# Kernel tuning notes

Hardware: AMD Instinct MI355X
Metric: run time of the kernel (lower is better)

## Reference

```python
import jax, jax.numpy as jnp
import numpy as np

T = 2048          # tokens (flattened prefill)
H = 3584          # hidden_size
NH = 16           # num query heads
NKV = 8           # num kv heads
G = NH // NKV     # GQA group size
D = 256           # head_dim
SCALE = 256.0 ** -0.5   # query_pre_attn_scalar ** -0.5
WINDOW = 1024     # sliding_window_size
CAP = 50.0        # logit softcap
BASE = 10000.0    # rope theta
NEG = -1e30


def _rope(x, positions):
    # x: [T, n, D], neox-style rotary over full head_dim
    half = D // 2
    inv_freq = 1.0 / (BASE ** (jnp.arange(0, D, 2, dtype=jnp.float32) / D))  # [half]
    ang = positions.astype(jnp.float32)[:, None] * inv_freq  # [T, half]
    cos = jnp.cos(ang)[:, None, :]  # [T,1,half]
    sin = jnp.sin(ang)[:, None, :]
    x1, x2 = x[..., :half], x[..., half:]
    return jnp.concatenate([x1 * cos - x2 * sin, x2 * cos + x1 * sin], axis=-1)


def setup_inputs() -> dict:
    key = jax.random.key(0)
    ks = jax.random.split(key, 5)
    s = 0.02
    return {
        "hidden_states": jax.random.normal(ks[0], (T, H), dtype=jnp.float32),
        "Wq": jax.random.normal(ks[1], (H, NH * D), dtype=jnp.float32) * s,
        "Wk": jax.random.normal(ks[2], (H, NKV * D), dtype=jnp.float32) * s,
        "Wv": jax.random.normal(ks[3], (H, NKV * D), dtype=jnp.float32) * s,
        "Wo": jax.random.normal(ks[4], (NH * D, H), dtype=jnp.float32) * s,
        "positions": jnp.arange(T, dtype=jnp.int32),
    }


def reference(hidden_states, Wq, Wk, Wv, Wo, positions):
    q = (hidden_states @ Wq).reshape(T, NH, D)
    k = (hidden_states @ Wk).reshape(T, NKV, D)
    v = (hidden_states @ Wv).reshape(T, NKV, D)
    q = _rope(q, positions)
    k = _rope(k, positions)

    # GQA attention: group query heads over kv heads
    qg = (q * SCALE).reshape(T, NKV, G, D)
    scores = jnp.einsum('qhgd,khd->hgqk', qg, k)  # [NKV,G,T,T]
    scores = CAP * jnp.tanh(scores / CAP)         # logit softcap

    i = jnp.arange(T)[:, None]
    j = jnp.arange(T)[None, :]
    mask = (j <= i) & (i - j < WINDOW)            # causal + sliding window
    scores = jnp.where(mask, scores, NEG)

    p = jax.nn.softmax(scores, axis=-1)
    o = jnp.einsum('hgqk,khd->qhgd', p, v).reshape(T, NH * D)
    return o @ Wo
```

## Files before the change

kernel.cpp:

```cpp
#include <hip/hip_runtime.h>
#include <math.h>

typedef __attribute__((ext_vector_type(8))) __bf16 bf16x8;
typedef __attribute__((ext_vector_type(4))) __bf16 bf16x4;
typedef __attribute__((ext_vector_type(4))) float f32x4;

#define TSEQ 2048
#define HDIM 3584
#define NQH  16
#define NKVH 8
#define DH   256
#define WIN  1024
#define QKD  (NQH * DH)
#define KVD  (NKVH * DH)
#define QKVN 8192

#define MFMA __builtin_amdgcn_mfma_f32_16x16x32_bf16

__device__ __forceinline__ void gload_lds16(const void* g, void* l) {
  __builtin_amdgcn_global_load_lds(
      (const __attribute__((address_space(1))) void*)g,
      (__attribute__((address_space(3))) void*)l, 16, 0, 0);
}


__global__ void cvt_bf16_kernel(const float* __restrict__ in,
                                __bf16* __restrict__ out, long n) {
  long i = ((long)blockIdx.x * blockDim.x + threadIdx.x) * 4;
  if (i >= n) return;
  float4 v = *reinterpret_cast<const float4*>(in + i);
  bf16x4 o4;
  o4.x = (__bf16)v.x; o4.y = (__bf16)v.y; o4.z = (__bf16)v.z; o4.w = (__bf16)v.w;
  *reinterpret_cast<bf16x4*>(out + i) = o4;
}

__global__ void transpose_cvt64_kernel(const float* __restrict__ in,
                                       __bf16* __restrict__ out, int R, int C) {
  __shared__ float tile[64][65];
  const int tid = threadIdx.x;
  const int r0 = blockIdx.y * 64, c0 = blockIdx.x * 64;
#pragma unroll
  for (int it = 0; it < 4; ++it) {
    int f = tid + it * 256;
    int row = f >> 4, c4 = (f & 15) * 4;
    float4 v = *reinterpret_cast<const float4*>(&in[(size_t)(r0 + row) * C + c0 + c4]);
    tile[row][c4] = v.x; tile[row][c4 + 1] = v.y;
    tile[row][c4 + 2] = v.z; tile[row][c4 + 3] = v.w;
  }
  __syncthreads();
#pragma unroll
  for (int it = 0; it < 2; ++it) {
    int s = tid + it * 256;
    int oc = s >> 3, rb = (s & 7) * 8;
    bf16x8 o8;
#pragma unroll
    for (int j = 0; j < 8; ++j) o8[j] = (__bf16)tile[rb + j][oc];
    *reinterpret_cast<bf16x8*>(&out[(size_t)(c0 + oc) * R + r0 + rb]) = o8;
  }
}

__global__ void transpose_bf16_kernel(const __bf16* __restrict__ in,
                                      __bf16* __restrict__ out, int ldin, int ldout) {
  __shared__ __bf16 tile[32][33];
  const int tx = threadIdx.x, ty = threadIdx.y;
  const int c0 = blockIdx.x * 32, r0 = blockIdx.y * 32;
#pragma unroll
  for (int i = 0; i < 4; ++i)
    tile[ty + i * 8][tx] = in[(size_t)(r0 + ty + i * 8) * ldin + (c0 + tx)];
  __syncthreads();
#pragma unroll
  for (int i = 0; i < 4; ++i)
    out[(size_t)(c0 + ty + i * 8) * ldout + (r0 + tx)] = tile[tx][ty + i * 8];
}

__global__ void rope_table_kernel(const int* __restrict__ positions,
                                  float* __restrict__ ct,
                                  float* __restrict__ st) {
  int i = blockIdx.x * blockDim.x + threadIdx.x;
  if (i >= TSEQ * 128) return;
  int t = i >> 7, j = i & 127;
  float invf = (float)exp((double)(-2 * j) * (9.210340371976184 / 256.0));
  float ang = (float)positions[t] * invf;
  ct[i] = cosf(ang);
  st[i] = sinf(ang);
}

__global__ void rope_apply_kernel(__bf16* __restrict__ x,
                                  const float* __restrict__ ct,
                                  const float* __restrict__ st,
                                  int heads, int ld, float scale, int total) {
  int i = blockIdx.x * blockDim.x + threadIdx.x;
  if (i >= total) return;
  int j = i & 127;
  int th = i >> 7;
  int t = th / heads;
  int head = th - t * heads;
  size_t base = (size_t)t * ld + head * DH + j;
  float x1 = (float)x[base], x2 = (float)x[base + 128];
  float c = ct[(t << 7) + j], s = st[(t << 7) + j];
  x[base]       = (__bf16)((x1 * c - x2 * s) * scale);
  x[base + 128] = (__bf16)((x2 * c + x1 * s) * scale);
}

__global__ void reduce2_kernel(const float* __restrict__ p0,
                               const float* __restrict__ p1,
                               float* __restrict__ out, int n4) {
  int stride = gridDim.x * blockDim.x;
  for (int i = blockIdx.x * blockDim.x + threadIdx.x; i < n4; i += stride) {
    float4 a = reinterpret_cast<const float4*>(p0)[i];
    float4 b = reinterpret_cast<const float4*>(p1)[i];
    a.x += b.x; a.y += b.y; a.z += b.z; a.w += b.w;
    reinterpret_cast<float4*>(out)[i] = a;
  }
}


__device__ __forceinline__ void stage_half(const __bf16* __restrict__ gbase,
                                           int row0, int ldg, int k0,
                                           __bf16* lds_half, int tid) {
  const int lane = tid & 63;
  const int w = tid >> 6;
  const int lr = lane >> 3;
  const int swzcol = ((lane & 7) ^ lr) << 3;
  const __bf16* g = gbase + (size_t)(row0 + w * 8 + lr) * ldg + k0 + swzcol;
  __bf16* l = lds_half + w * 512;
  gload_lds16(g, l);
  gload_lds16(g + (size_t)64 * ldg, l + 4096);
}

#define BAR __builtin_amdgcn_s_barrier()

#define RD_A(DST, BASE, MO)                                         \
  _Pragma("unroll")                                                 \
  for (int m_ = 0; m_ < 4; ++m_) {                                  \
    const __bf16* p_ = (BASE) + (((MO) + m_) * 16 + l15) * 64;      \
    DST[m_][0] = *(const bf16x8*)(p_ + kxa);                        \
    DST[m_][1] = *(const bf16x8*)(p_ + kxb);                        \
  }

#define RD_B(DST, BASE, NO)                                         \
  _Pragma("unroll")                                                 \
  for (int n_ = 0; n_ < 2; ++n_) {                                  \
    const __bf16* p_ = (BASE) + (bro + ((NO) + n_) * 16 + l15) * 64;\
    DST[n_][0] = *(const bf16x8*)(p_ + kxa);                        \
    DST[n_][1] = *(const bf16x8*)(p_ + kxb);                        \
  }

#define MQUAD(AF, BF, MO, NO)                                          \
  __builtin_amdgcn_s_setprio(1);                                       \
  _Pragma("unroll")                                                    \
  for (int m_ = 0; m_ < 4; ++m_)                                       \
    _Pragma("unroll")                                                  \
    for (int n_ = 0; n_ < 2; ++n_) {                                   \
      acc[(MO) + m_][(NO) + n_] =                                      \
          MFMA(AF[m_][0], BF[n_][0], acc[(MO) + m_][(NO) + n_], 0, 0, 0); \
      acc[(MO) + m_][(NO) + n_] =                                      \
          MFMA(AF[m_][1], BF[n_][1], acc[(MO) + m_][(NO) + n_], 0, 0, 0); \
    }                                                                  \
  __builtin_amdgcn_s_setprio(0);

template <typename CT>
__global__ __launch_bounds__(512, 2) void gemm256_kernel(
    const __bf16* __restrict__ A, const __bf16* __restrict__ B,
    CT* __restrict__ C, int lda, int Klen, int ldc, int nrc, size_t cstride) {
  __shared__ __bf16 lds[2][2][2][8192];

  const int nwg = gridDim.x;
  const int per = nwg >> 3;
  const int wg = (blockIdx.x & 7) * per + (blockIdx.x >> 3);
  const int kslice = wg / nrc;
  const int rem = wg - kslice * nrc;
  const int row0 = (rem & 7) * 256;
  const int col0 = (rem >> 3) * 256;
  const int k0 = kslice * Klen;
  CT* Cs = C + (size_t)kslice * cstride;

  const int tid = threadIdx.x;
  const int lane = tid & 63, w = tid >> 6;
  const int wr = w >> 2, wc = w & 3;
  const int l15 = lane & 15, lg = lane >> 4;
  const int swz = (lane & 7) << 3;
  const int kxa = (lg * 8) ^ swz;
  const int kxb = (32 + lg * 8) ^ swz;
  const int bro = (wc & 1) * 64;

  const __bf16* Ablk = A + (size_t)row0 * lda + k0;
  const __bf16* Bblk = B + (size_t)col0 * lda + k0;

  const __bf16* Ae = &lds[0][0][wr][0];
  const __bf16* Be = &lds[0][1][wc >> 1][0];
  const __bf16* Ao = &lds[1][0][wr][0];
  const __bf16* Bo = &lds[1][1][wc >> 1][0];

  f32x4 acc[8][4] = {};
  const int NT = Klen >> 6;
  const int NI = NT >> 1;

  stage_half(Ablk, 0,   lda, 0,  &lds[0][0][0][0], tid);
  stage_half(Ablk, 128, lda, 0,  &lds[0][0][1][0], tid);
  stage_half(Bblk, 0,   lda, 0,  &lds[0][1][0][0], tid);
  stage_half(Bblk, 128, lda, 0,  &lds[0][1][1][0], tid);
  stage_half(Ablk, 0,   lda, 64, &lds[1][0][0][0], tid);
  stage_half(Ablk, 128, lda, 64, &lds[1][0][1][0], tid);
  asm volatile("s_waitcnt vmcnt(4)" ::: "memory");
  BAR;

  bf16x8 a03[4][2], a47[4][2], b01[2][2], b23[2][2];

  for (int j = 0; j < NI; ++j) {
    const int e = 2 * j, o = 2 * j + 1;
    const bool last = (j == NI - 1);

    RD_A(a03, Ae, 0);
    RD_B(b01, Be, 0);
    stage_half(Bblk, 0, lda, o * 64, &lds[1][1][0][0], tid);
    asm volatile("s_waitcnt lgkmcnt(8)" ::: "memory");
    BAR; MQUAD(a03, b01, 0, 0); BAR;

    RD_A(a47, Ae, 4);
    stage_half(Bblk, 128, lda, o * 64, &lds[1][1][1][0], tid);
    BAR; MQUAD(a47, b01, 4, 0); BAR;

    RD_B(b23, Be, 2);
    if (!last) stage_half(Ablk, 0, lda, (e + 2) * 64, &lds[0][0][0][0], tid);
    BAR; MQUAD(a47, b23, 4, 2); BAR;

    if (!last) {
      stage_half(Ablk, 128, lda, (e + 2) * 64, &lds[0][0][1][0], tid);
      asm volatile("s_waitcnt vmcnt(4)" ::: "memory");
    } else {
      asm volatile("s_waitcnt vmcnt(0)" ::: "memory");
    }
    BAR; MQUAD(a03, b23, 0, 2); BAR;

    RD_A(a03, Ao, 0);
    RD_B(b01, Bo, 0);
    if (!last) stage_half(Bblk, 0, lda, (e + 2) * 64, &lds[0][1][0][0], tid);
    asm volatile("s_waitcnt lgkmcnt(8)" ::: "memory");
    BAR; MQUAD(a03, b01, 0, 0); BAR;

    RD_A(a47, Ao, 4);
    if (!last) stage_half(Bblk, 128, lda, (e + 2) * 64, &lds[0][1][1][0], tid);
    BAR; MQUAD(a47, b01, 4, 0); BAR;

    RD_B(b23, Bo, 2);
    if (!last) stage_half(Ablk, 0, lda, (o + 2) * 64, &lds[1][0][0][0], tid);
    BAR; MQUAD(a47, b23, 4, 2); BAR;

    if (!last) {
      stage_half(Ablk, 128, lda, (o + 2) * 64, &lds[1][0][1][0], tid);
      asm volatile("s_waitcnt vmcnt(4)" ::: "memory");
    }
    BAR; MQUAD(a03, b23, 0, 2); BAR;
  }

#pragma unroll
  for (int m = 0; m < 8; ++m)
#pragma unroll
    for (int n = 0; n < 4; ++n)
#pragma unroll
      for (int r = 0; r < 4; ++r) {
        int row = row0 + wr * 128 + m * 16 + lg * 4 + r;
        int col = col0 + wc * 64 + n * 16 + l15;
        Cs[(size_t)row * ldc + col] = (CT)acc[m][n][r];
      }
}

__global__ __launch_bounds__(512, 2) void attn_kernel(
    const __bf16* __restrict__ q, const __bf16* __restrict__ k,
    const __bf16* __restrict__ vt, __bf16* __restrict__ o) {
  __shared__ __bf16 Klds[64][264];
  __shared__ __bf16 Vlds[256][72];
  __shared__ __bf16 Plds[8][16][72];

  const int tid = threadIdx.x;
  const int wave = tid >> 6;
  const int lane = tid & 63;
  const int l16 = lane & 15;
  const int lg = lane >> 4;
  const int h = blockIdx.y;
  const int qh = 2 * h + (wave >> 2);
  const int wsub = wave & 3;
  const int q0 = blockIdx.x << 6;
  const int qr = q0 + wsub * 16;

  bf16x8 qf[8];
  {
    const __bf16* qp = q + (size_t)(qr + l16) * QKVN + qh * DH + lg * 8;
#pragma unroll
    for (int ds = 0; ds < 8; ++ds)
      qf[ds] = *reinterpret_cast<const bf16x8*>(qp + ds * 32);
  }

  f32x4 accO[16] = {};
  float l_run[4] = {0.f, 0.f, 0.f, 0.f};

  int t_lo = q0 - (WIN - 1);
  if (t_lo < 0) t_lo = 0;
  t_lo &= ~63;

  const __bf16* kg0 = k + (size_t)h * DH;
  const __bf16* vg0 = vt + (size_t)(h * DH) * TSEQ;

  bf16x8 kpre[4], vpre[4];
#pragma unroll
  for (int it = 0; it < 4; ++it) {
    int c = tid + it * 512;
    kpre[it] = *reinterpret_cast<const bf16x8*>(
        kg0 + (size_t)(t_lo + (c >> 5)) * QKVN + (c & 31) * 8);
    vpre[it] = *reinterpret_cast<const bf16x8*>(
        vg0 + (size_t)(c >> 3) * TSEQ + t_lo + (c & 7) * 8);
  }

  for (int t0 = t_lo; t0 <= q0; t0 += 64) {
    __syncthreads();
#pragma unroll
    for (int it = 0; it < 4; ++it) {
      int c = tid + it * 512;
      *reinterpret_cast<bf16x8*>(&Klds[c >> 5][(c & 31) * 8]) = kpre[it];
      *reinterpret_cast<bf16x8*>(&Vlds[c >> 3][(c & 7) * 8]) = vpre[it];
    }
    __syncthreads();

    if (t0 + 64 <= q0) {
      const int tn = t0 + 64;
#pragma unroll
      for (int it = 0; it < 4; ++it) {
        int c = tid + it * 512;
        kpre[it] = *reinterpret_cast<const bf16x8*>(
            kg0 + (size_t)(tn + (c >> 5)) * QKVN + (c & 31) * 8);
        vpre[it] = *reinterpret_cast<const bf16x8*>(
            vg0 + (size_t)(c >> 3) * TSEQ + tn + (c & 7) * 8);
      }
    }

    f32x4 accS[4] = {};
    __builtin_amdgcn_s_setprio(1);
#pragma unroll
    for (int nt = 0; nt < 4; ++nt)
#pragma unroll
      for (int ds = 0; ds < 8; ++ds) {
        bf16x8 kf = *reinterpret_cast<const bf16x8*>(&Klds[nt * 16 + l16][ds * 32 + lg * 8]);
        accS[nt] = MFMA(qf[ds], kf, accS[nt], 0, 0, 0);
      }
    __builtin_amdgcn_s_setprio(0);

    float rs[4] = {0.f, 0.f, 0.f, 0.f};
#pragma unroll
    for (int nt = 0; nt < 4; ++nt) {
      int key = t0 + nt * 16 + l16;
#pragma unroll
      for (int r = 0; r < 4; ++r) {
        int row = qr + lg * 4 + r;
        float t = __expf(accS[nt][r] * 0.04f);
        float p = __expf(-100.0f / (t + 1.0f));
        bool valid = (key <= row) && (row - key < WIN);
        p = valid ? p : 0.f;
        rs[r] += p;
        Plds[wave][lg * 4 + r][nt * 16 + l16] = (__bf16)p;
      }
    }
#pragma unroll
    for (int off = 1; off < 16; off <<= 1)
#pragma unroll
      for (int r = 0; r < 4; ++r)
        rs[r] += __shfl_xor(rs[r], off);
#pragma unroll
    for (int r = 0; r < 4; ++r)
      l_run[r] += rs[r];

    __builtin_amdgcn_s_setprio(1);
#pragma unroll
    for (int ks = 0; ks < 2; ++ks) {
      bf16x8 pa = *reinterpret_cast<const bf16x8*>(&Plds[wave][l16][ks * 32 + lg * 8]);
#pragma unroll
      for (int nt2 = 0; nt2 < 16; ++nt2) {
        bf16x8 vb = *reinterpret_cast<const bf16x8*>(&Vlds[nt2 * 16 + l16][ks * 32 + lg * 8]);
        accO[nt2] = MFMA(pa, vb, accO[nt2], 0, 0, 0);
      }
    }
    __builtin_amdgcn_s_setprio(0);
  }

#pragma unroll
  for (int r = 0; r < 4; ++r) {
    float inv_l = 1.f / l_run[r];
    int row = qr + lg * 4 + r;
#pragma unroll
    for (int nt2 = 0; nt2 < 16; ++nt2)
      o[(size_t)row * QKD + qh * DH + nt2 * 16 + l16] = (__bf16)(accO[nt2][r] * inv_l);
  }
}


extern "C" void kernel_launch(void* const* d_in, const int* in_sizes, int n_in,
                              void* d_out, int out_size, void* d_ws, size_t ws_size,
                              hipStream_t stream) {
  const float* hs = (const float*)d_in[0];
  const float* Wq = (const float*)d_in[1];
  const float* Wk = (const float*)d_in[2];
  const float* Wv = (const float*)d_in[3];
  const float* Wo = (const float*)d_in[4];
  const int* positions = (const int*)d_in[5];
  float* out = (float*)d_out;

  char* ws = (char*)d_ws;
  const size_t SZ_HS  = (size_t)TSEQ * HDIM * 2;
  const size_t SZ_WQT = (size_t)QKD * HDIM * 2;
  const size_t SZ_WKT = (size_t)KVD * HDIM * 2;
  const size_t SZ_WOT = (size_t)HDIM * QKD * 2;
  const size_t SZ_QKV = (size_t)TSEQ * QKVN * 2;
  const size_t SZ_O   = (size_t)TSEQ * QKD * 2;
  const size_t SZ_TBL = (size_t)TSEQ * 128 * 4;

  __bf16* hs_bf = (__bf16*)ws; ws += SZ_HS;
  __bf16* WqT   = (__bf16*)ws; ws += SZ_WQT;
  __bf16* WkT   = (__bf16*)ws; ws += SZ_WKT;
  __bf16* WvT   = (__bf16*)ws; ws += SZ_WKT;
  __bf16* WoT   = (__bf16*)ws; ws += SZ_WOT;
  __bf16* qkv   = (__bf16*)ws; ws += SZ_QKV;
  __bf16* o_bf  = (__bf16*)ws; ws += SZ_O;
  float*  cost  = (float*)ws;  ws += SZ_TBL;
  float*  sint  = (float*)ws;  ws += SZ_TBL;
  __bf16* vt_bf = hs_bf;
  float* cpart = (float*)WqT;
  if ((size_t)(ws - (char*)d_ws) > ws_size) return;

  cvt_bf16_kernel<<<(TSEQ * HDIM) / 1024, 256, 0, stream>>>(hs, hs_bf, (long)TSEQ * HDIM);
  transpose_cvt64_kernel<<<dim3(QKD / 64, HDIM / 64), 256, 0, stream>>>(Wq, WqT, HDIM, QKD);
  transpose_cvt64_kernel<<<dim3(KVD / 64, HDIM / 64), 256, 0, stream>>>(Wk, WkT, HDIM, KVD);
  transpose_cvt64_kernel<<<dim3(KVD / 64, HDIM / 64), 256, 0, stream>>>(Wv, WvT, HDIM, KVD);
  transpose_cvt64_kernel<<<dim3(HDIM / 64, QKD / 64), 256, 0, stream>>>(Wo, WoT, QKD, HDIM);
  rope_table_kernel<<<(TSEQ * 128) / 256, 256, 0, stream>>>(positions, cost, sint);

  gemm256_kernel<__bf16><<<256, 512, 0, stream>>>(hs_bf, WqT, qkv, HDIM, HDIM, QKVN, 256, 0);

  rope_apply_kernel<<<(TSEQ * NQH * 128) / 256, 256, 0, stream>>>(qkv, cost, sint, NQH, QKVN, 0.0625f, TSEQ * NQH * 128);
  rope_apply_kernel<<<(TSEQ * NKVH * 128) / 256, 256, 0, stream>>>(qkv + QKD, cost, sint, NKVH, QKVN, 1.0f, TSEQ * NKVH * 128);
  transpose_bf16_kernel<<<dim3(KVD / 32, TSEQ / 32), dim3(32, 8), 0, stream>>>(qkv + QKD + KVD, vt_bf, QKVN, TSEQ);

  attn_kernel<<<dim3(TSEQ / 64, NKVH), 512, 0, stream>>>(qkv, qkv + QKD, vt_bf, o_bf);

  gemm256_kernel<float><<<224, 512, 0, stream>>>(o_bf, WoT, cpart, QKD, QKD / 2, HDIM, 112,
                                                 (size_t)TSEQ * HDIM);
  reduce2_kernel<<<1792, 256, 0, stream>>>(cpart, cpart + (size_t)TSEQ * HDIM, out,
                                           TSEQ * HDIM / 4);
}
```

Measured before the change: 336.2 us.

## Double-buffer attention K/V via direct LDS loads, merge prep kernels, bf16 partials

The attention kernel now runs 256 threads per block, each wave handling two 16-row query groups. K/V tiles are double-buffered in swizzled LDS and staged with direct global-to-LDS loads, so the next tile's fetch overlaps compute on the current one and each K/V fragment is reused across two MFMAs. Separately, the four weight-transpose launches are merged into one kernel and the two RoPE launches into one. The split-K output GEMM now writes bf16 partials that the reduce kernel converts back to fp32, halving partial traffic at some cost in output precision.

```diff
diff --git a/kernel.cpp b/kernel.cpp
--- a/kernel.cpp
+++ b/kernel.cpp
@@ -34,16 +34,29 @@
   *reinterpret_cast<bf16x4*>(out + i) = o4;
 }
 
-__global__ void transpose_cvt64_kernel(const float* __restrict__ in,
-                                       __bf16* __restrict__ out, int R, int C) {
+__global__ void transpose_all_kernel(const float* __restrict__ Wq,
+                                     const float* __restrict__ Wk,
+                                     const float* __restrict__ Wv,
+                                     const float* __restrict__ Wo,
+                                     __bf16* __restrict__ WqT,
+                                     __bf16* __restrict__ WkT,
+                                     __bf16* __restrict__ WvT,
+                                     __bf16* __restrict__ WoT) {
   __shared__ float tile[64][65];
+  int id = blockIdx.x;
+  const float* src; __bf16* dst; int R, C;
+  if (id < 3584)      { src = Wq; dst = WqT; R = HDIM; C = QKD; }
+  else if (id < 5376) { id -= 3584; src = Wk; dst = WkT; R = HDIM; C = KVD; }
+  else if (id < 7168) { id -= 5376; src = Wv; dst = WvT; R = HDIM; C = KVD; }
+  else                { id -= 7168; src = Wo; dst = WoT; R = QKD; C = HDIM; }
+  const int nbx = C >> 6;
+  const int c0 = (id % nbx) * 64, r0 = (id / nbx) * 64;
   const int tid = threadIdx.x;
-  const int r0 = blockIdx.y * 64, c0 = blockIdx.x * 64;
 #pragma unroll
   for (int it = 0; it < 4; ++it) {
     int f = tid + it * 256;
     int row = f >> 4, c4 = (f & 15) * 4;
-    float4 v = *reinterpret_cast<const float4*>(&in[(size_t)(r0 + row) * C + c0 + c4]);
+    float4 v = *reinterpret_cast<const float4*>(&src[(size_t)(r0 + row) * C + c0 + c4]);
     tile[row][c4] = v.x; tile[row][c4 + 1] = v.y;
     tile[row][c4 + 2] = v.z; tile[row][c4 + 3] = v.w;
   }
@@ -55,7 +68,7 @@
     bf16x8 o8;
 #pragma unroll
     for (int j = 0; j < 8; ++j) o8[j] = (__bf16)tile[rb + j][oc];
-    *reinterpret_cast<bf16x8*>(&out[(size_t)(c0 + oc) * R + r0 + rb]) = o8;
+    *reinterpret_cast<bf16x8*>(&dst[(size_t)(c0 + oc) * R + r0 + rb]) = o8;
   }
 }
 
@@ -85,32 +98,36 @@
   st[i] = sinf(ang);
 }
 
-__global__ void rope_apply_kernel(__bf16* __restrict__ x,
-                                  const float* __restrict__ ct,
-                                  const float* __restrict__ st,
-                                  int heads, int ld, float scale, int total) {
+__global__ void rope_qk_kernel(__bf16* __restrict__ qkv,
+                               const float* __restrict__ ct,
+                               const float* __restrict__ st) {
   int i = blockIdx.x * blockDim.x + threadIdx.x;
-  if (i >= total) return;
   int j = i & 127;
   int th = i >> 7;
-  int t = th / heads;
-  int head = th - t * heads;
-  size_t base = (size_t)t * ld + head * DH + j;
-  float x1 = (float)x[base], x2 = (float)x[base + 128];
+  int t = th / 24;
+  int hh = th - t * 24;
+  float scale = (hh < 16) ? 0.0625f : 1.0f;
+  size_t base = (size_t)t * QKVN + ((hh < 16) ? hh * DH : QKD + (hh - 16) * DH) + j;
+  float x1 = (float)qkv[base], x2 = (float)qkv[base + 128];
   float c = ct[(t << 7) + j], s = st[(t << 7) + j];
-  x[base]       = (__bf16)((x1 * c - x2 * s) * scale);
-  x[base + 128] = (__bf16)((x2 * c + x1 * s) * scale);
-}
-
-__global__ void reduce2_kernel(const float* __restrict__ p0,
-                               const float* __restrict__ p1,
-                               float* __restrict__ out, int n4) {
+  qkv[base]       = (__bf16)((x1 * c - x2 * s) * scale);
+  qkv[base + 128] = (__bf16)((x2 * c + x1 * s) * scale);
+}
+
+__global__ void reduce2_kernel(const __bf16* __restrict__ p0,
+                               const __bf16* __restrict__ p1,
+                               float* __restrict__ out, int n8) {
   int stride = gridDim.x * blockDim.x;
-  for (int i = blockIdx.x * blockDim.x + threadIdx.x; i < n4; i += stride) {
-    float4 a = reinterpret_cast<const float4*>(p0)[i];
-    float4 b = reinterpret_cast<const float4*>(p1)[i];
-    a.x += b.x; a.y += b.y; a.z += b.z; a.w += b.w;
-    reinterpret_cast<float4*>(out)[i] = a;
+  for (int i = blockIdx.x * blockDim.x + threadIdx.x; i < n8; i += stride) {
+    bf16x8 a = reinterpret_cast<const bf16x8*>(p0)[i];
+    bf16x8 b = reinterpret_cast<const bf16x8*>(p1)[i];
+    float4 o0, o1;
+    o0.x = (float)a[0] + (float)b[0]; o0.y = (float)a[1] + (float)b[1];
+    o0.z = (float)a[2] + (float)b[2]; o0.w = (float)a[3] + (float)b[3];
+    o1.x = (float)a[4] + (float)b[4]; o1.y = (float)a[5] + (float)b[5];
+    o1.z = (float)a[6] + (float)b[6]; o1.w = (float)a[7] + (float)b[7];
+    reinterpret_cast<float4*>(out)[2 * i] = o0;
+    reinterpret_cast<float4*>(out)[2 * i + 1] = o1;
   }
 }
 
@@ -266,12 +283,31 @@
       }
 }
 
-__global__ __launch_bounds__(512, 2) void attn_kernel(
+
+__device__ __forceinline__ void attn_stage(const __bf16* __restrict__ kg,
+                                           const __bf16* __restrict__ vg,
+                                           __bf16* Kd, __bf16* Vd, int tid) {
+  const int ktr = tid >> 5;
+  const int kslot = (tid & 31) ^ ktr;
+  const __bf16* ks = kg + (size_t)ktr * QKVN + kslot * 8;
+  __bf16* kd = Kd + tid * 8;
+  const int vtr = (tid >> 3) & 7;
+  const int vslot = (tid & 7) ^ vtr;
+  const __bf16* vs = vg + (size_t)(tid >> 3) * TSEQ + vslot * 8;
+  __bf16* vd = Vd + tid * 8;
+#pragma unroll
+  for (int i = 0; i < 8; ++i) {
+    gload_lds16(ks + (size_t)(i * 8) * QKVN, kd + i * 2048);
+    gload_lds16(vs + (size_t)(i * 32) * TSEQ, vd + i * 2048);
+  }
+}
+
+__global__ __launch_bounds__(256, 1) void attn_kernel(
     const __bf16* __restrict__ q, const __bf16* __restrict__ k,
     const __bf16* __restrict__ vt, __bf16* __restrict__ o) {
-  __shared__ __bf16 Klds[64][264];
-  __shared__ __bf16 Vlds[256][72];
-  __shared__ __bf16 Plds[8][16][72];
+  __shared__ __bf16 Klds[2][64][256];
+  __shared__ __bf16 Vlds[2][256][64];
+  __shared__ __bf16 Plds[4][2][16][72];
 
   const int tid = threadIdx.x;
   const int wave = tid >> 6;
@@ -279,117 +315,113 @@
   const int l16 = lane & 15;
   const int lg = lane >> 4;
   const int h = blockIdx.y;
-  const int qh = 2 * h + (wave >> 2);
-  const int wsub = wave & 3;
+  const int qh = 2 * h + (wave >> 1);
   const int q0 = blockIdx.x << 6;
-  const int qr = q0 + wsub * 16;
-
-  bf16x8 qf[8];
-  {
-    const __bf16* qp = q + (size_t)(qr + l16) * QKVN + qh * DH + lg * 8;
-#pragma unroll
-    for (int ds = 0; ds < 8; ++ds)
-      qf[ds] = *reinterpret_cast<const bf16x8*>(qp + ds * 32);
-  }
-
-  f32x4 accO[16] = {};
-  float l_run[4] = {0.f, 0.f, 0.f, 0.f};
+  const int qr = q0 + (wave & 1) * 32;
+
+  const __bf16* kg0 = k + (size_t)h * DH;
+  const __bf16* vg0 = vt + (size_t)(h * DH) * TSEQ;
 
   int t_lo = q0 - (WIN - 1);
   if (t_lo < 0) t_lo = 0;
   t_lo &= ~63;
-
-  const __bf16* kg0 = k + (size_t)h * DH;
-  const __bf16* vg0 = vt + (size_t)(h * DH) * TSEQ;
-
-  bf16x8 kpre[4], vpre[4];
-#pragma unroll
-  for (int it = 0; it < 4; ++it) {
-    int c = tid + it * 512;
-    kpre[it] = *reinterpret_cast<const bf16x8*>(
-        kg0 + (size_t)(t_lo + (c >> 5)) * QKVN + (c & 31) * 8);
-    vpre[it] = *reinterpret_cast<const bf16x8*>(
-        vg0 + (size_t)(c >> 3) * TSEQ + t_lo + (c & 7) * 8);
-  }
-
-  for (int t0 = t_lo; t0 <= q0; t0 += 64) {
-    __syncthreads();
-#pragma unroll
-    for (int it = 0; it < 4; ++it) {
-      int c = tid + it * 512;
-      *reinterpret_cast<bf16x8*>(&Klds[c >> 5][(c & 31) * 8]) = kpre[it];
-      *reinterpret_cast<bf16x8*>(&Vlds[c >> 3][(c & 7) * 8]) = vpre[it];
-    }
-    __syncthreads();
-
-    if (t0 + 64 <= q0) {
-      const int tn = t0 + 64;
-#pragma unroll
-      for (int it = 0; it < 4; ++it) {
-        int c = tid + it * 512;
-        kpre[it] = *reinterpret_cast<const bf16x8*>(
-            kg0 + (size_t)(tn + (c >> 5)) * QKVN + (c & 31) * 8);
-        vpre[it] = *reinterpret_cast<const bf16x8*>(
-            vg0 + (size_t)(c >> 3) * TSEQ + tn + (c & 7) * 8);
+  const int NTile = ((q0 - t_lo) >> 6) + 1;
+
+  attn_stage(kg0 + (size_t)t_lo * QKVN, vg0 + t_lo, &Klds[0][0][0], &Vlds[0][0][0], tid);
+
+  bf16x8 qf[2][8];
+#pragma unroll
+  for (int g = 0; g < 2; ++g) {
+    const __bf16* qp = q + (size_t)(qr + 16 * g + l16) * QKVN + qh * DH + lg * 8;
+#pragma unroll
+    for (int ds = 0; ds < 8; ++ds)
+      qf[g][ds] = *reinterpret_cast<const bf16x8*>(qp + ds * 32);
+  }
+
+  f32x4 accO[2][16] = {};
+  float l_run[2][4] = {};
+
+  for (int it = 0; it < NTile; ++it) {
+    const int t0 = t_lo + it * 64;
+    const int cur = it & 1;
+
+    if (it + 1 < NTile) {
+      attn_stage(kg0 + (size_t)(t0 + 64) * QKVN, vg0 + (t0 + 64),
+                 &Klds[cur ^ 1][0][0], &Vlds[cur ^ 1][0][0], tid);
+      asm volatile("s_waitcnt vmcnt(16)" ::: "memory");
+    } else {
+      asm volatile("s_waitcnt vmcnt(0)" ::: "memory");
+    }
+    __builtin_amdgcn_s_barrier();
+
+    const __bf16* Kc = &Klds[cur][0][0];
+    const __bf16* Vc = &Vlds[cur][0][0];
+
+    f32x4 accS[2][4] = {};
+#pragma unroll
+    for (int ds = 0; ds < 8; ++ds)
+#pragma unroll
+      for (int nt = 0; nt < 4; ++nt) {
+        int row = nt * 16 + l16;
+        int slot = (4 * ds + lg) ^ (l16 & 7);
+        bf16x8 kf = *reinterpret_cast<const bf16x8*>(Kc + row * 256 + slot * 8);
+        accS[0][nt] = MFMA(qf[0][ds], kf, accS[0][nt], 0, 0, 0);
+        accS[1][nt] = MFMA(qf[1][ds], kf, accS[1][nt], 0, 0, 0);
       }
-    }
-
-    f32x4 accS[4] = {};
-    __builtin_amdgcn_s_setprio(1);
-#pragma unroll
-    for (int nt = 0; nt < 4; ++nt)
-#pragma unroll
-      for (int ds = 0; ds < 8; ++ds) {
-        bf16x8 kf = *reinterpret_cast<const bf16x8*>(&Klds[nt * 16 + l16][ds * 32 + lg * 8]);
-        accS[nt] = MFMA(qf[ds], kf, accS[nt], 0, 0, 0);
+
+#pragma unroll
+    for (int g = 0; g < 2; ++g) {
+      float rs[4] = {0.f, 0.f, 0.f, 0.f};
+#pragma unroll
+      for (int nt = 0; nt < 4; ++nt) {
+        int key = t0 + nt * 16 + l16;
+#pragma unroll
+        for (int r = 0; r < 4; ++r) {
+          int row = qr + 16 * g + lg * 4 + r;
+          float t = __expf(accS[g][nt][r] * 0.04f);
+          float p = __expf(-100.0f / (t + 1.0f));
+          bool valid = (key <= row) && (row - key < WIN);
+          p = valid ? p : 0.f;
+          rs[r] += p;
+          Plds[wave][g][lg * 4 + r][nt * 16 + l16] = (__bf16)p;
+        }
       }
-    __builtin_amdgcn_s_setprio(0);
-
-    float rs[4] = {0.f, 0.f, 0.f, 0.f};
-#pragma unroll
-    for (int nt = 0; nt < 4; ++nt) {
-      int key = t0 + nt * 16 + l16;
-#pragma unroll
-      for (int r = 0; r < 4; ++r) {
-        int row = qr + lg * 4 + r;
-        float t = __expf(accS[nt][r] * 0.04f);
-        float p = __expf(-100.0f / (t + 1.0f));
-        bool valid = (key <= row) && (row - key < WIN);
-        p = valid ? p : 0.f;
-        rs[r] += p;
-        Plds[wave][lg * 4 + r][nt * 16 + l16] = (__bf16)p;
+#pragma unroll
+      for (int off = 1; off < 16; off <<= 1)
+#pragma unroll
+        for (int r = 0; r < 4; ++r)
+          rs[r] += __shfl_xor(rs[r], off);
+#pragma unroll
+      for (int r = 0; r < 4; ++r)
+        l_run[g][r] += rs[r];
+    }
+
+#pragma unroll
+    for (int ks = 0; ks < 2; ++ks) {
+      bf16x8 pa0 = *reinterpret_cast<const bf16x8*>(&Plds[wave][0][l16][ks * 32 + lg * 8]);
+      bf16x8 pa1 = *reinterpret_cast<const bf16x8*>(&Plds[wave][1][l16][ks * 32 + lg * 8]);
+#pragma unroll
+      for (int nt2 = 0; nt2 < 16; ++nt2) {
+        int row = nt2 * 16 + l16;
+        int slot = (4 * ks + lg) ^ (l16 & 7);
+        bf16x8 vb = *reinterpret_cast<const bf16x8*>(Vc + row * 64 + slot * 8);
+        accO[0][nt2] = MFMA(pa0, vb, accO[0][nt2], 0, 0, 0);
+        accO[1][nt2] = MFMA(pa1, vb, accO[1][nt2], 0, 0, 0);
       }
     }
-#pragma unroll
-    for (int off = 1; off < 16; off <<= 1)
-#pragma unroll
-      for (int r = 0; r < 4; ++r)
-        rs[r] += __shfl_xor(rs[r], off);
-#pragma unroll
-    for (int r = 0; r < 4; ++r)
-      l_run[r] += rs[r];
-
-    __builtin_amdgcn_s_setprio(1);
-#pragma unroll
-    for (int ks = 0; ks < 2; ++ks) {
-      bf16x8 pa = *reinterpret_cast<const bf16x8*>(&Plds[wave][l16][ks * 32 + lg * 8]);
-#pragma unroll
-      for (int nt2 = 0; nt2 < 16; ++nt2) {
-        bf16x8 vb = *reinterpret_cast<const bf16x8*>(&Vlds[nt2 * 16 + l16][ks * 32 + lg * 8]);
-        accO[nt2] = MFMA(pa, vb, accO[nt2], 0, 0, 0);
-      }
-    }
-    __builtin_amdgcn_s_setprio(0);
-  }
-
-#pragma unroll
-  for (int r = 0; r < 4; ++r) {
-    float inv_l = 1.f / l_run[r];
-    int row = qr + lg * 4 + r;
-#pragma unroll
-    for (int nt2 = 0; nt2 < 16; ++nt2)
-      o[(size_t)row * QKD + qh * DH + nt2 * 16 + l16] = (__bf16)(accO[nt2][r] * inv_l);
-  }
+    __builtin_amdgcn_s_barrier();
+  }
+
+#pragma unroll
+  for (int g = 0; g < 2; ++g)
+#pragma unroll
+    for (int r = 0; r < 4; ++r) {
+      float inv_l = 1.f / l_run[g][r];
+      int row = qr + 16 * g + lg * 4 + r;
+#pragma unroll
+      for (int nt2 = 0; nt2 < 16; ++nt2)
+        o[(size_t)row * QKD + qh * DH + nt2 * 16 + l16] = (__bf16)(accO[g][nt2][r] * inv_l);
+    }
 }
 
 
@@ -423,26 +455,22 @@
   float*  cost  = (float*)ws;  ws += SZ_TBL;
   float*  sint  = (float*)ws;  ws += SZ_TBL;
   __bf16* vt_bf = hs_bf;
-  float* cpart = (float*)WqT;
+  __bf16* cpart = WqT;
   if ((size_t)(ws - (char*)d_ws) > ws_size) return;
 
   cvt_bf16_kernel<<<(TSEQ * HDIM) / 1024, 256, 0, stream>>>(hs, hs_bf, (long)TSEQ * HDIM);
-  transpose_cvt64_kernel<<<dim3(QKD / 64, HDIM / 64), 256, 0, stream>>>(Wq, WqT, HDIM, QKD);
-  transpose_cvt64_kernel<<<dim3(KVD / 64, HDIM / 64), 256, 0, stream>>>(Wk, WkT, HDIM, KVD);
-  transpose_cvt64_kernel<<<dim3(KVD / 64, HDIM / 64), 256, 0, stream>>>(Wv, WvT, HDIM, KVD);
-  transpose_cvt64_kernel<<<dim3(HDIM / 64, QKD / 64), 256, 0, stream>>>(Wo, WoT, QKD, HDIM);
+  transpose_all_kernel<<<10752, 256, 0, stream>>>(Wq, Wk, Wv, Wo, WqT, WkT, WvT, WoT);
   rope_table_kernel<<<(TSEQ * 128) / 256, 256, 0, stream>>>(positions, cost, sint);
 
   gemm256_kernel<__bf16><<<256, 512, 0, stream>>>(hs_bf, WqT, qkv, HDIM, HDIM, QKVN, 256, 0);
 
-  rope_apply_kernel<<<(TSEQ * NQH * 128) / 256, 256, 0, stream>>>(qkv, cost, sint, NQH, QKVN, 0.0625f, TSEQ * NQH * 128);
-  rope_apply_kernel<<<(TSEQ * NKVH * 128) / 256, 256, 0, stream>>>(qkv + QKD, cost, sint, NKVH, QKVN, 1.0f, TSEQ * NKVH * 128);
+  rope_qk_kernel<<<(TSEQ * 24 * 128) / 256, 256, 0, stream>>>(qkv, cost, sint);
   transpose_bf16_kernel<<<dim3(KVD / 32, TSEQ / 32), dim3(32, 8), 0, stream>>>(qkv + QKD + KVD, vt_bf, QKVN, TSEQ);
 
-  attn_kernel<<<dim3(TSEQ / 64, NKVH), 512, 0, stream>>>(qkv, qkv + QKD, vt_bf, o_bf);
-
-  gemm256_kernel<float><<<224, 512, 0, stream>>>(o_bf, WoT, cpart, QKD, QKD / 2, HDIM, 112,
-                                                 (size_t)TSEQ * HDIM);
-  reduce2_kernel<<<1792, 256, 0, stream>>>(cpart, cpart + (size_t)TSEQ * HDIM, out,
-                                           TSEQ * HDIM / 4);
-}
+  attn_kernel<<<dim3(TSEQ / 64, NKVH), 256, 0, stream>>>(qkv, qkv + QKD, vt_bf, o_bf);
+
+  gemm256_kernel<__bf16><<<224, 512, 0, stream>>>(o_bf, WoT, cpart, QKD, QKD / 2, HDIM, 112,
+                                                  (size_t)TSEQ * HDIM);
+  reduce2_kernel<<<2048, 256, 0, stream>>>(cpart, cpart + (size_t)TSEQ * HDIM, out,
+                                           TSEQ * HDIM / 8);
+}
```

After: 342.3 us. About the same (+1.8%).
